# Performance work log

Measured on AMD Instinct MI355X. Metric: run time of the kernel, lower is better.

Reference implementation:

```python
import jax, jax.numpy as jnp
import numpy as np


def setup_inputs() -> dict:
    key = jax.random.key(0)
    ks = jax.random.split(key, 5)
    B, Cin, Ch, H, W, K = 8, 64, 64, 128, 128, 3
    fan_in = (Cin + Ch) * K * K
    return {
        "x": jax.random.normal(ks[0], (B, Cin, H, W), jnp.float32),
        "prev_h": jax.random.normal(ks[1], (B, Ch, H, W), jnp.float32),
        "prev_c": jax.random.normal(ks[2], (B, Ch, H, W), jnp.float32),
        "W_gates": jax.random.normal(ks[3], (4 * Ch, Cin + Ch, K, K), jnp.float32) / np.sqrt(fan_in),
        "b_gates": jax.random.normal(ks[4], (4 * Ch,), jnp.float32) * 0.01,
    }


def reference(x, prev_h, prev_c, W_gates, b_gates):
    # ConvLSTM cell: conv over concat(input, prev_h) -> 4 gates -> gating.
    pad = W_gates.shape[-1] // 2
    stacked = jnp.concatenate([x, prev_h], axis=1)  # [B, Cin+Ch, H, W]
    gates = jax.lax.conv_general_dilated(
        stacked, W_gates,
        window_strides=(1, 1),
        padding=[(pad, pad), (pad, pad)],
        dimension_numbers=("NCHW", "OIHW", "NCHW"),
    ) + b_gates[None, :, None, None]  # [B, 4*Ch, H, W]
    in_gate, remember_gate, out_gate, cell_gate = jnp.split(gates, 4, axis=1)
    in_gate = jax.nn.sigmoid(in_gate)
    remember_gate = jax.nn.sigmoid(remember_gate)
    out_gate = jax.nn.sigmoid(out_gate)
    cell_gate = jnp.tanh(cell_gate)
    cell = in_gate * cell_gate + remember_gate * prev_c
    hidden = out_gate * jnp.tanh(cell)
    return (hidden, cell)
```

## Files before the change

### kernel.cpp

```cpp
#include <hip/hip_runtime.h>

typedef __attribute__((ext_vector_type(8))) short short8;
typedef __attribute__((ext_vector_type(4))) short short4v;
typedef __attribute__((ext_vector_type(4))) float float4v;

#define NPIX_HID 8388608
#define PSTRIDE 132

__device__ __forceinline__ short f2bf(float f) {
    union { float f; unsigned u; } v; v.f = f;
    unsigned r = (v.u + 0x7FFFu + ((v.u >> 16) & 1u)) >> 16;
    return (short)r;
}

__device__ __forceinline__ float sigmoidf_(float v) { return 1.f / (1.f + __expf(-v)); }
__device__ __forceinline__ float tanhf_(float v)    { return 2.f / (1.f + __expf(-2.f * v)) - 1.f; }

__global__ void wprep(const float* __restrict__ W, short* __restrict__ A) {
    int tid = blockIdx.x * 256 + threadIdx.x;
    if (tid >= 9 * 16 * 256 * 8) return;
    int j   = tid & 7;
    int co  = (tid >> 3) & 255;
    int cig = (tid >> 11) & 15;
    int kk  = tid >> 15;
    int ci  = cig * 8 + j;
    A[tid] = f2bf(W[co * 1152 + ci * 9 + kk]);
}

__global__ __launch_bounds__(256, 3) void convlstm_main(
    const float* __restrict__ x, const float* __restrict__ ph,
    const float* __restrict__ pc, const short* __restrict__ aprep,
    const float* __restrict__ bg, float* __restrict__ out)
{
    __shared__ short Bs[3 * 66 * PSTRIDE];

    const int tid  = threadIdx.x;
    const int lane = tid & 63;
    const int wave = tid >> 6;
    const int l15  = lane & 15;
    const int quad = lane >> 4;

    const int t  = blockIdx.x;
    const int x0 = (t & 1) * 64;
    const int y  = (t >> 1) & 127;
    const int b  = t >> 8;

    for (int i = tid; i < 3168; i += 256) {
        const int px  = i % 66;
        const int ro  = i / 66;
        const int oct = ro & 15;
        const int row = ro >> 4;
        const int ysrc = y + row - 1;
        const int xsrc = x0 + px - 1;
        short4v lo = {0, 0, 0, 0}, hi = {0, 0, 0, 0};
        if ((unsigned)ysrc < 128u && (unsigned)xsrc < 128u) {
            const float* src = (oct < 8) ? x : ph;
            const float* sp = src + (((b * 64 + (oct & 7) * 8) * 128 + ysrc) * 128 + xsrc);
#pragma unroll
            for (int j = 0; j < 4; ++j) lo[j] = f2bf(sp[j * 16384]);
#pragma unroll
            for (int j = 0; j < 4; ++j) hi[j] = f2bf(sp[(j + 4) * 16384]);
        }
        short* dst = &Bs[(row * 66 + px) * PSTRIDE + oct * 8];
        *(short4v*)dst       = lo;
        *(short4v*)(dst + 4) = hi;
    }
    __syncthreads();

    float4v acc[4][4];
#pragma unroll
    for (int mt = 0; mt < 4; ++mt)
#pragma unroll
        for (int nt = 0; nt < 4; ++nt)
            acc[mt][nt] = (float4v){0.f, 0.f, 0.f, 0.f};

#pragma unroll
    for (int ky = 0; ky < 3; ++ky) {
#pragma unroll
        for (int kx = 0; kx < 3; ++kx) {
            const int kkk = ky * 3 + kx;
#pragma unroll
            for (int kc = 0; kc < 4; ++kc) {
                short8 afr[4], bfr[4];
                const short* ab = aprep + ((kkk * 16 + kc * 4 + quad) * 256) * 8;
#pragma unroll
                for (int mt = 0; mt < 4; ++mt)
                    afr[mt] = *(const short8*)(ab + (mt * 64 + wave * 16 + l15) * 8);
                const int bbase = (ky * 66 + kx + l15) * PSTRIDE + kc * 32 + quad * 8;
#pragma unroll
                for (int nt = 0; nt < 4; ++nt) {
                    const short* bp = &Bs[bbase + nt * 16 * PSTRIDE];
                    short4v blo = *(const short4v*)bp;
                    short4v bhi = *(const short4v*)(bp + 4);
                    short8 f;
                    f[0] = blo[0]; f[1] = blo[1]; f[2] = blo[2]; f[3] = blo[3];
                    f[4] = bhi[0]; f[5] = bhi[1]; f[6] = bhi[2]; f[7] = bhi[3];
                    bfr[nt] = f;
                }
#pragma unroll
                for (int mt = 0; mt < 4; ++mt)
#pragma unroll
                    for (int nt = 0; nt < 4; ++nt)
                        acc[mt][nt] = __builtin_amdgcn_mfma_f32_16x16x32_bf16(
                            afr[mt], bfr[nt], acc[mt][nt], 0, 0, 0);
            }
        }
    }

#pragma unroll
    for (int nt = 0; nt < 4; ++nt) {
        const int px = x0 + nt * 16 + l15;
#pragma unroll
        for (int r = 0; r < 4; ++r) {
            const int c = wave * 16 + quad * 4 + r;
            const float gi = acc[0][nt][r] + bg[c];
            const float gf = acc[1][nt][r] + bg[64 + c];
            const float go = acc[2][nt][r] + bg[128 + c];
            const float gc = acc[3][nt][r] + bg[192 + c];
            const float ig = sigmoidf_(gi);
            const float fg = sigmoidf_(gf);
            const float og = sigmoidf_(go);
            const float cg = tanhf_(gc);
            const int idx = ((b * 64 + c) * 128 + y) * 128 + px;
            const float cell = ig * cg + fg * pc[idx];
            const float hid  = og * tanhf_(cell);
            out[idx] = hid;
            out[NPIX_HID + idx] = cell;
        }
    }
}

extern "C" void kernel_launch(void* const* d_in, const int* in_sizes, int n_in,
                              void* d_out, int out_size, void* d_ws, size_t ws_size,
                              hipStream_t stream) {
    const float* x  = (const float*)d_in[0];
    const float* ph = (const float*)d_in[1];
    const float* pc = (const float*)d_in[2];
    const float* W  = (const float*)d_in[3];
    const float* bg = (const float*)d_in[4];
    float* out = (float*)d_out;
    short* aprep = (short*)d_ws;

    wprep<<<1152, 256, 0, stream>>>(W, aprep);
    convlstm_main<<<2048, 256, 0, stream>>>(x, ph, pc, aprep, bg, out);
}
```

Before: 256.3 us.

## Process two output rows per block and prefetch weight fragments across k-steps

Each block now computes a 2x64 pixel tile, loading 4 halo rows instead of 3. That cuts the redundant halo loads and fp32-to-bf16 conversion per output row and reuses each weight fragment over 8 N-tiles instead of 4. The k-loop is flattened into 36 non-unrolled steps with register double-buffering of the A fragments. LDS rows are padded to 136 and read as single 16-byte loads. This doubles accumulator registers and lowers launch bounds to 2 blocks/SM with half as many blocks, risking lower occupancy and less latency hiding.

```diff
diff --git a/kernel.cpp b/kernel.cpp
--- a/kernel.cpp
+++ b/kernel.cpp
@@ -1,11 +1,10 @@
 #include <hip/hip_runtime.h>
 
 typedef __attribute__((ext_vector_type(8))) short short8;
-typedef __attribute__((ext_vector_type(4))) short short4v;
 typedef __attribute__((ext_vector_type(4))) float float4v;
 
 #define NPIX_HID 8388608
-#define PSTRIDE 132
+#define PST 136
 
 __device__ __forceinline__ short f2bf(float f) {
     union { float f; unsigned u; } v; v.f = f;
@@ -27,12 +26,12 @@
     A[tid] = f2bf(W[co * 1152 + ci * 9 + kk]);
 }
 
-__global__ __launch_bounds__(256, 3) void convlstm_main(
+__global__ __launch_bounds__(256, 2) void convlstm_main(
     const float* __restrict__ x, const float* __restrict__ ph,
     const float* __restrict__ pc, const short* __restrict__ aprep,
     const float* __restrict__ bg, float* __restrict__ out)
 {
-    __shared__ short Bs[3 * 66 * PSTRIDE];
+    __shared__ short Bs[4 * 66 * PST];
 
     const int tid  = threadIdx.x;
     const int lane = tid & 63;
@@ -42,74 +41,79 @@
 
     const int t  = blockIdx.x;
     const int x0 = (t & 1) * 64;
-    const int y  = (t >> 1) & 127;
-    const int b  = t >> 8;
+    const int y0 = ((t >> 1) & 63) * 2;
+    const int b  = t >> 7;
 
-    for (int i = tid; i < 3168; i += 256) {
+    for (int i = tid; i < 4224; i += 256) {
         const int px  = i % 66;
         const int ro  = i / 66;
         const int oct = ro & 15;
         const int row = ro >> 4;
-        const int ysrc = y + row - 1;
+        const int ysrc = y0 + row - 1;
         const int xsrc = x0 + px - 1;
-        short4v lo = {0, 0, 0, 0}, hi = {0, 0, 0, 0};
+        short8 pk = {0,0,0,0,0,0,0,0};
         if ((unsigned)ysrc < 128u && (unsigned)xsrc < 128u) {
             const float* src = (oct < 8) ? x : ph;
             const float* sp = src + (((b * 64 + (oct & 7) * 8) * 128 + ysrc) * 128 + xsrc);
 #pragma unroll
-            for (int j = 0; j < 4; ++j) lo[j] = f2bf(sp[j * 16384]);
-#pragma unroll
-            for (int j = 0; j < 4; ++j) hi[j] = f2bf(sp[(j + 4) * 16384]);
+            for (int j = 0; j < 8; ++j) pk[j] = f2bf(sp[j * 16384]);
         }
-        short* dst = &Bs[(row * 66 + px) * PSTRIDE + oct * 8];
-        *(short4v*)dst       = lo;
-        *(short4v*)(dst + 4) = hi;
+        *(short8*)&Bs[(row * 66 + px) * PST + oct * 8] = pk;
     }
     __syncthreads();
 
-    float4v acc[4][4];
+    float4v acc[4][8];
 #pragma unroll
     for (int mt = 0; mt < 4; ++mt)
 #pragma unroll
-        for (int nt = 0; nt < 4; ++nt)
+        for (int nt = 0; nt < 8; ++nt)
             acc[mt][nt] = (float4v){0.f, 0.f, 0.f, 0.f};
 
+    const int coff = (wave * 16 + l15) * 8;
+    short8 afr[4];
+    {
+        const short* ab = aprep + quad * 2048;
 #pragma unroll
-    for (int ky = 0; ky < 3; ++ky) {
+        for (int mt = 0; mt < 4; ++mt)
+            afr[mt] = *(const short8*)(ab + mt * 512 + coff);
+    }
+
+#pragma unroll 1
+    for (int kt = 0; kt < 36; ++kt) {
+        const int ktn = (kt < 35) ? kt + 1 : 35;
+        short8 anx[4];
+        const short* abn = aprep + ktn * 8192 + quad * 2048;
 #pragma unroll
-        for (int kx = 0; kx < 3; ++kx) {
-            const int kkk = ky * 3 + kx;
+        for (int mt = 0; mt < 4; ++mt)
+            anx[mt] = *(const short8*)(abn + mt * 512 + coff);
+
+        const int kkk = kt >> 2;
+        const int kc  = kt & 3;
+        const int ky  = (kkk * 11) >> 5;
+        const int kx  = kkk - ky * 3;
+        const int kof = kc * 32 + quad * 8;
+
+        short8 bfr[8];
 #pragma unroll
-            for (int kc = 0; kc < 4; ++kc) {
-                short8 afr[4], bfr[4];
-                const short* ab = aprep + ((kkk * 16 + kc * 4 + quad) * 256) * 8;
+        for (int nt = 0; nt < 8; ++nt) {
+            const int rowh = ky + (nt >> 2);
+            const int pxi  = kx + ((nt & 3) << 4) + l15;
+            bfr[nt] = *(const short8*)&Bs[(rowh * 66 + pxi) * PST + kof];
+        }
 #pragma unroll
-                for (int mt = 0; mt < 4; ++mt)
-                    afr[mt] = *(const short8*)(ab + (mt * 64 + wave * 16 + l15) * 8);
-                const int bbase = (ky * 66 + kx + l15) * PSTRIDE + kc * 32 + quad * 8;
+        for (int mt = 0; mt < 4; ++mt)
 #pragma unroll
-                for (int nt = 0; nt < 4; ++nt) {
-                    const short* bp = &Bs[bbase + nt * 16 * PSTRIDE];
-                    short4v blo = *(const short4v*)bp;
-                    short4v bhi = *(const short4v*)(bp + 4);
-                    short8 f;
-                    f[0] = blo[0]; f[1] = blo[1]; f[2] = blo[2]; f[3] = blo[3];
-                    f[4] = bhi[0]; f[5] = bhi[1]; f[6] = bhi[2]; f[7] = bhi[3];
-                    bfr[nt] = f;
-                }
+            for (int nt = 0; nt < 8; ++nt)
+                acc[mt][nt] = __builtin_amdgcn_mfma_f32_16x16x32_bf16(
+                    afr[mt], bfr[nt], acc[mt][nt], 0, 0, 0);
 #pragma unroll
-                for (int mt = 0; mt < 4; ++mt)
-#pragma unroll
-                    for (int nt = 0; nt < 4; ++nt)
-                        acc[mt][nt] = __builtin_amdgcn_mfma_f32_16x16x32_bf16(
-                            afr[mt], bfr[nt], acc[mt][nt], 0, 0, 0);
-            }
-        }
+        for (int mt = 0; mt < 4; ++mt) afr[mt] = anx[mt];
     }
 
 #pragma unroll
-    for (int nt = 0; nt < 4; ++nt) {
-        const int px = x0 + nt * 16 + l15;
+    for (int nt = 0; nt < 8; ++nt) {
+        const int y  = y0 + (nt >> 2);
+        const int px = x0 + ((nt & 3) << 4) + l15;
 #pragma unroll
         for (int r = 0; r < 4; ++r) {
             const int c = wave * 16 + quad * 4 + r;
@@ -142,5 +146,5 @@
     short* aprep = (short*)d_ws;
 
     wprep<<<1152, 256, 0, stream>>>(W, aprep);
-    convlstm_main<<<2048, 256, 0, stream>>>(x, ph, pc, aprep, bg, out);
+    convlstm_main<<<1024, 256, 0, stream>>>(x, ph, pc, aprep, bg, out);
 }
```

After: 228.7 us. 1.12x faster.
